# Kernel optimization log

Measured on AMD Instinct MI355X. Metric: run time of the kernel, lower is better.

The kernel has to match this reference:

```python
import jax, jax.numpy as jnp
import numpy as np

M, N, D, P = 1024, 4096, 128, 3072
H = N // D


def setup_inputs() -> dict:
    key = jax.random.key(0)
    ks = jax.random.split(key, 6)
    X = jax.random.normal(ks[0], (M, N), dtype=jnp.float32)
    W_q = jax.random.normal(ks[1], (N, N), dtype=jnp.float32) * 0.02
    W_k = jax.random.normal(ks[2], (N, N), dtype=jnp.float32) * 0.02
    W_v = jax.random.normal(ks[3], (N, N), dtype=jnp.float32) * 0.02
    cache_K = jax.random.normal(ks[4], (H, P, D), dtype=jnp.float32)
    cache_V = jax.random.normal(ks[5], (H, P, D), dtype=jnp.float32)
    return {"X": X, "W_q": W_q, "W_k": W_k, "W_v": W_v,
            "cache_K": cache_K, "cache_V": cache_V}


def _rms_norm(t):
    # RMS over last dim, no eps, no learned scale (matches source)
    var = jnp.mean(t * t, axis=-1, keepdims=True)
    return t * jax.lax.rsqrt(var)


def reference(X, W_q, W_k, W_v, cache_K, cache_V):
    # QKV projections: [M, N] -> [H, M, D]
    q = (X @ W_q).reshape(M, H, D).transpose(1, 0, 2)
    k = (X @ W_k).reshape(M, H, D).transpose(1, 0, 2)
    v = (X @ W_v).reshape(M, H, D).transpose(1, 0, 2)

    q = _rms_norm(q)
    k = _rms_norm(k)

    # KV-cache concat along sequence dim: [H, P+M, D]
    k_cache = jnp.concatenate([cache_K[:, :P, :], k], axis=1)
    v_cache = jnp.concatenate([cache_V[:, :P, :], v], axis=1)

    # Non-causal prefill attention, sm_scale = 1.0
    scores = jnp.einsum('hmd,hnd->hmn', q, k_cache)  # [H, M, P+M]
    attn = jax.nn.softmax(scores, axis=-1)
    out = jnp.einsum('hmn,hnd->hmd', attn, v_cache)  # [H, M, D]

    return out.transpose(1, 0, 2).reshape(M, N)
```

## Files before the change

kernel.cpp:

```cpp
#include <hip/hip_runtime.h>

#define MM 1024
#define NN 4096
#define DD 128
#define HH 32
#define PP 3072
#define LL 4096

typedef __attribute__((ext_vector_type(8))) short short8;
typedef __attribute__((ext_vector_type(4))) float f32x4;

__device__ __forceinline__ float bf2f(short b) {
  union { unsigned u; float f; } c;
  c.u = ((unsigned)(unsigned short)b) << 16;
  return c.f;
}

__device__ __forceinline__ short f2bf(float f) {
  union { float f; unsigned u; } c; c.f = f;
  unsigned r = c.u + 0x7FFFu + ((c.u >> 16) & 1u);
  return (short)(r >> 16);
}

struct bf2 { short hi, lo; };
__device__ __forceinline__ bf2 split2(float x) {
  bf2 r;
  r.hi = f2bf(x);
  r.lo = f2bf(x - bf2f(r.hi));
  return r;
}

__device__ __forceinline__ short8 cvt8(const float* __restrict__ p) {
  const f32x4 a = *(const f32x4*)p;
  const f32x4 b = *(const f32x4*)(p + 4);
  short8 r;
  r[0] = f2bf(a[0]); r[1] = f2bf(a[1]); r[2] = f2bf(a[2]); r[3] = f2bf(a[3]);
  r[4] = f2bf(b[0]); r[5] = f2bf(b[1]); r[6] = f2bf(b[2]); r[7] = f2bf(b[3]);
  return r;
}

__global__ __launch_bounds__(256) void split_x(
    const float* __restrict__ in, short* __restrict__ oh,
    short* __restrict__ ol, int n8)
{
  int i = blockIdx.x * blockDim.x + threadIdx.x;
  if (i >= n8) return;
  const float* p = in + (size_t)i * 8;
  f32x4 a = *(const f32x4*)p, b = *(const f32x4*)(p + 4);
  short8 h, l;
  #pragma unroll
  for (int j = 0; j < 4; ++j) {
    bf2 ra = split2(a[j]); h[j] = ra.hi; l[j] = ra.lo;
    bf2 rb = split2(b[j]); h[4 + j] = rb.hi; l[4 + j] = rb.lo;
  }
  *(short8*)(oh + (size_t)i * 8) = h;
  *(short8*)(ol + (size_t)i * 8) = l;
}

__global__ __launch_bounds__(256) void gemm_qk_split(
    const short* __restrict__ Xhi, const short* __restrict__ Xlo,
    const float* __restrict__ Wq, const float* __restrict__ Wk,
    float* __restrict__ Oq, float* __restrict__ Ok)
{
  const int z = blockIdx.z;
  const float* __restrict__ W = (z == 0) ? Wq : Wk;
  float* __restrict__ O = (z == 0) ? Oq : Ok;

  const int n0 = blockIdx.x * 128;
  const int m0 = blockIdx.y * 128;
  const int t  = threadIdx.x;
  const int wave = t >> 6;
  const int lane = t & 63;
  const int ln   = lane & 15;
  const int quad = lane >> 4;
  const int q8   = quad * 8;
  const int wm = (wave >> 1) * 64;
  const int wn = (wave & 1) * 64;

  __shared__ short Ah[128 * 72];
  __shared__ short Al[128 * 72];
  __shared__ short Bh[64 * 136];
  __shared__ short Bl[64 * 136];

  f32x4 acc[4][4];
  #pragma unroll
  for (int mi = 0; mi < 4; ++mi)
    #pragma unroll
    for (int ni = 0; ni < 4; ++ni)
      acc[mi][ni] = (f32x4){0.f, 0.f, 0.f, 0.f};

  const int ar = t >> 3, ac = (t & 7) * 8;
  const int bk = t >> 4, bn = (t & 15) * 8;

  for (int kt = 0; kt < 4096; kt += 64) {
    #pragma unroll
    for (int i = 0; i < 4; ++i) {
      int r = i * 32 + ar;
      size_t off = (size_t)(m0 + r) * 4096 + kt + ac;
      *(short8*)(Ah + r * 72 + ac) = *(const short8*)(Xhi + off);
      *(short8*)(Al + r * 72 + ac) = *(const short8*)(Xlo + off);
    }
    #pragma unroll
    for (int i = 0; i < 4; ++i) {
      int kr = i * 16 + bk;
      const float* wp = W + (size_t)(kt + kr) * 4096 + n0 + bn;
      f32x4 x0 = *(const f32x4*)wp, x1 = *(const f32x4*)(wp + 4);
      short8 hh, ll;
      #pragma unroll
      for (int j = 0; j < 4; ++j) {
        bf2 r0 = split2(x0[j]); hh[j] = r0.hi; ll[j] = r0.lo;
        bf2 r1 = split2(x1[j]); hh[4 + j] = r1.hi; ll[4 + j] = r1.lo;
      }
      int cb = (bn >> 3) ^ (kr >> 3);
      *(short8*)(Bh + kr * 136 + cb * 8) = hh;
      *(short8*)(Bl + kr * 136 + cb * 8) = ll;
    }
    __syncthreads();
    #pragma unroll
    for (int kk = 0; kk < 64; kk += 32) {
      short8 afh[4], afl[4];
      #pragma unroll
      for (int mi = 0; mi < 4; ++mi) {
        int ro = (wm + mi * 16 + ln) * 72 + kk + q8;
        afh[mi] = *(const short8*)(Ah + ro);
        afl[mi] = *(const short8*)(Al + ro);
      }
      #pragma unroll
      for (int ni = 0; ni < 4; ++ni) {
        short8 bh, bl;
        #pragma unroll
        for (int j = 0; j < 8; ++j) {
          int k = kk + q8 + j;
          int idx = k * 136 + ((((wn + ni * 16 + ln) >> 3) ^ (k >> 3)) << 3) + (ln & 7);
          bh[j] = Bh[idx];
          bl[j] = Bl[idx];
        }
        #pragma unroll
        for (int mi = 0; mi < 4; ++mi) {
          acc[mi][ni] = __builtin_amdgcn_mfma_f32_16x16x32_bf16(afh[mi], bh, acc[mi][ni], 0, 0, 0);
          acc[mi][ni] = __builtin_amdgcn_mfma_f32_16x16x32_bf16(afh[mi], bl, acc[mi][ni], 0, 0, 0);
          acc[mi][ni] = __builtin_amdgcn_mfma_f32_16x16x32_bf16(afl[mi], bh, acc[mi][ni], 0, 0, 0);
        }
      }
    }
    __syncthreads();
  }

  #pragma unroll
  for (int mi = 0; mi < 4; ++mi)
    #pragma unroll
    for (int ni = 0; ni < 4; ++ni)
      #pragma unroll
      for (int r = 0; r < 4; ++r) {
        int row = m0 + wm + mi * 16 + quad * 4 + r;
        int col = n0 + wn + ni * 16 + ln;
        O[(size_t)row * 4096 + col] = acc[mi][ni][r];
      }
}

__global__ __launch_bounds__(256) void gemm_v(
    const short* __restrict__ Xhi, const float* __restrict__ Wv,
    short* __restrict__ Ov)
{
  const int n0 = blockIdx.x * 128;
  const int m0 = blockIdx.y * 128;
  const int t  = threadIdx.x;
  const int wave = t >> 6;
  const int lane = t & 63;
  const int ln   = lane & 15;
  const int quad = lane >> 4;
  const int q8   = quad * 8;
  const int wm = (wave >> 1) * 64;
  const int wn = (wave & 1) * 64;

  __shared__ short Ah[128 * 72];
  __shared__ short Bh[64 * 136];

  f32x4 acc[4][4];
  #pragma unroll
  for (int mi = 0; mi < 4; ++mi)
    #pragma unroll
    for (int ni = 0; ni < 4; ++ni)
      acc[mi][ni] = (f32x4){0.f, 0.f, 0.f, 0.f};

  const int ar = t >> 3, ac = (t & 7) * 8;
  const int bk = t >> 4, bn = (t & 15) * 8;

  for (int kt = 0; kt < 4096; kt += 64) {
    #pragma unroll
    for (int i = 0; i < 4; ++i) {
      int r = i * 32 + ar;
      *(short8*)(Ah + r * 72 + ac) =
          *(const short8*)(Xhi + (size_t)(m0 + r) * 4096 + kt + ac);
    }
    #pragma unroll
    for (int i = 0; i < 4; ++i) {
      int kr = i * 16 + bk;
      int cb = (bn >> 3) ^ (kr >> 3);
      *(short8*)(Bh + kr * 136 + cb * 8) =
          cvt8(Wv + (size_t)(kt + kr) * 4096 + n0 + bn);
    }
    __syncthreads();
    #pragma unroll
    for (int kk = 0; kk < 64; kk += 32) {
      short8 afh[4];
      #pragma unroll
      for (int mi = 0; mi < 4; ++mi)
        afh[mi] = *(const short8*)(Ah + (wm + mi * 16 + ln) * 72 + kk + q8);
      #pragma unroll
      for (int ni = 0; ni < 4; ++ni) {
        short8 bh;
        #pragma unroll
        for (int j = 0; j < 8; ++j) {
          int k = kk + q8 + j;
          int idx = k * 136 + ((((wn + ni * 16 + ln) >> 3) ^ (k >> 3)) << 3) + (ln & 7);
          bh[j] = Bh[idx];
        }
        #pragma unroll
        for (int mi = 0; mi < 4; ++mi)
          acc[mi][ni] = __builtin_amdgcn_mfma_f32_16x16x32_bf16(afh[mi], bh, acc[mi][ni], 0, 0, 0);
      }
    }
    __syncthreads();
  }

  #pragma unroll
  for (int mi = 0; mi < 4; ++mi)
    #pragma unroll
    for (int ni = 0; ni < 4; ++ni)
      #pragma unroll
      for (int r = 0; r < 4; ++r) {
        int row = m0 + wm + mi * 16 + quad * 4 + r;
        int col = n0 + wn + ni * 16 + ln;
        Ov[(size_t)row * 4096 + col] = f2bf(acc[mi][ni][r]);
      }
}

__global__ __launch_bounds__(256) void rmsnorm_f32(
    float* __restrict__ Q, float* __restrict__ K)
{
  float* __restrict__ buf = (blockIdx.y == 0) ? Q : K;
  const int m = blockIdx.x;
  const int t = threadIdx.x;
  const int head = t >> 3, li = t & 7;
  size_t base = (size_t)m * 4096 + head * 128 + li * 16;

  f32x4 a[4];
  float ss = 0.f;
  #pragma unroll
  for (int i = 0; i < 4; ++i) {
    a[i] = *(const f32x4*)(buf + base + i * 4);
    #pragma unroll
    for (int j = 0; j < 4; ++j) ss += a[i][j] * a[i][j];
  }
  #pragma unroll
  for (int d = 1; d < 8; d <<= 1) ss += __shfl_xor(ss, d, 64);
  float scale = rsqrtf(ss * (1.0f / 128.0f));
  #pragma unroll
  for (int i = 0; i < 4; ++i) {
    #pragma unroll
    for (int j = 0; j < 4; ++j) a[i][j] *= scale;
    *(f32x4*)(buf + base + i * 4) = a[i];
  }
}

__global__ __launch_bounds__(256) void attn(
    const float* __restrict__ Qf,
    const float* __restrict__ Kf,
    const short* __restrict__ Vb,
    const float* __restrict__ cK,
    const float* __restrict__ cV,
    float* __restrict__ Out)
{
  const int h  = blockIdx.y;
  const int m0 = blockIdx.x * 64;
  const int t  = threadIdx.x;
  const int w    = t >> 6;
  const int lane = t & 63;
  const int ln   = lane & 15;
  const int quad = lane >> 4;
  const int q8   = quad * 8;

  __shared__ short k_hi[64 * 136];
  __shared__ short k_lo[64 * 136];
  __shared__ short v_s[64 * 136];
  __shared__ short p_s[64 * 72];
  __shared__ float a_l[64], l_l[64];

  short8 qh[4], ql[4];
  {
    int qrow = m0 + w * 16 + ln;
    #pragma unroll
    for (int dc = 0; dc < 4; ++dc) {
      const float* qp = Qf + (size_t)qrow * 4096 + h * 128 + dc * 32 + q8;
      f32x4 a = *(const f32x4*)qp, b = *(const f32x4*)(qp + 4);
      #pragma unroll
      for (int j = 0; j < 4; ++j) {
        bf2 ra = split2(a[j]); qh[dc][j] = ra.hi; ql[dc][j] = ra.lo;
        bf2 rb = split2(b[j]); qh[dc][4 + j] = rb.hi; ql[dc][4 + j] = rb.lo;
      }
    }
  }

  float m_st[4], l_st[4];
  #pragma unroll
  for (int r = 0; r < 4; ++r) { m_st[r] = -1e30f; l_st[r] = 0.f; }

  f32x4 oacc[4][2];
  #pragma unroll
  for (int ms = 0; ms < 4; ++ms)
    #pragma unroll
    for (int i = 0; i < 2; ++i)
      oacc[ms][i] = (f32x4){0.f, 0.f, 0.f, 0.f};

  for (int kb = 0; kb < LL; kb += 64) {
    #pragma unroll
    for (int i = 0; i < 2; ++i) {
      int kr = i * 32 + (t >> 3);
      int g  = kb + kr;
      int dc = (t & 7) * 16;
      const float* ks = (g < PP)
          ? cK + ((size_t)h * PP + g) * 128 + dc
          : Kf + (size_t)(g - PP) * 4096 + h * 128 + dc;
      f32x4 x0 = *(const f32x4*)ks,       x1 = *(const f32x4*)(ks + 4);
      f32x4 x2 = *(const f32x4*)(ks + 8), x3 = *(const f32x4*)(ks + 12);
      short8 h0, l0, h1, l1;
      #pragma unroll
      for (int j = 0; j < 4; ++j) {
        bf2 r0 = split2(x0[j]); h0[j] = r0.hi; l0[j] = r0.lo;
        bf2 r1 = split2(x1[j]); h0[4 + j] = r1.hi; l0[4 + j] = r1.lo;
        bf2 r2 = split2(x2[j]); h1[j] = r2.hi; l1[j] = r2.lo;
        bf2 r3 = split2(x3[j]); h1[4 + j] = r3.hi; l1[4 + j] = r3.lo;
      }
      *(short8*)(k_hi + kr * 136 + dc)     = h0;
      *(short8*)(k_hi + kr * 136 + dc + 8) = h1;
      *(short8*)(k_lo + kr * 136 + dc)     = l0;
      *(short8*)(k_lo + kr * 136 + dc + 8) = l1;

      short8 v0, v1;
      if (g < PP) {
        const float* vs = cV + ((size_t)h * PP + g) * 128 + dc;
        v0 = cvt8(vs); v1 = cvt8(vs + 8);
      } else {
        const short* vp = Vb + (size_t)(g - PP) * 4096 + h * 128 + dc;
        v0 = *(const short8*)vp; v1 = *(const short8*)(vp + 8);
      }
      int b0 = ((dc >> 3) + 0) ^ (kr >> 3);
      int b1 = ((dc >> 3) + 1) ^ (kr >> 3);
      *(short8*)(v_s + kr * 136 + b0 * 8) = v0;
      *(short8*)(v_s + kr * 136 + b1 * 8) = v1;
    }
    __syncthreads();

    f32x4 sacc[4];
    #pragma unroll
    for (int ni = 0; ni < 4; ++ni) sacc[ni] = (f32x4){0.f, 0.f, 0.f, 0.f};
    #pragma unroll
    for (int ni = 0; ni < 4; ++ni) {
      #pragma unroll
      for (int dc = 0; dc < 4; ++dc) {
        int ro = (ni * 16 + ln) * 136 + dc * 32 + q8;
        short8 kh = *(const short8*)(k_hi + ro);
        short8 kl = *(const short8*)(k_lo + ro);
        sacc[ni] = __builtin_amdgcn_mfma_f32_16x16x32_bf16(qh[dc], kh, sacc[ni], 0, 0, 0);
        sacc[ni] = __builtin_amdgcn_mfma_f32_16x16x32_bf16(qh[dc], kl, sacc[ni], 0, 0, 0);
        sacc[ni] = __builtin_amdgcn_mfma_f32_16x16x32_bf16(ql[dc], kh, sacc[ni], 0, 0, 0);
      }
    }

    float alpha[4];
    #pragma unroll
    for (int rr = 0; rr < 4; ++rr) {
      float mx = fmaxf(fmaxf(sacc[0][rr], sacc[1][rr]),
                       fmaxf(sacc[2][rr], sacc[3][rr]));
      #pragma unroll
      for (int d = 1; d < 16; d <<= 1) mx = fmaxf(mx, __shfl_xor(mx, d, 64));
      float mn = fmaxf(m_st[rr], mx);
      alpha[rr] = __expf(m_st[rr] - mn);
      float p0 = __expf(sacc[0][rr] - mn);
      float p1 = __expf(sacc[1][rr] - mn);
      float p2 = __expf(sacc[2][rr] - mn);
      float p3 = __expf(sacc[3][rr] - mn);
      float s = p0 + p1 + p2 + p3;
      #pragma unroll
      for (int d = 1; d < 16; d <<= 1) s += __shfl_xor(s, d, 64);
      l_st[rr] = l_st[rr] * alpha[rr] + s;
      m_st[rr] = mn;
      int prow = (w * 16 + quad * 4 + rr) * 72;
      p_s[prow + 0 * 16 + ln] = f2bf(p0);
      p_s[prow + 1 * 16 + ln] = f2bf(p1);
      p_s[prow + 2 * 16 + ln] = f2bf(p2);
      p_s[prow + 3 * 16 + ln] = f2bf(p3);
    }
    if (ln == 0) {
      #pragma unroll
      for (int rr = 0; rr < 4; ++rr) a_l[w * 16 + quad * 4 + rr] = alpha[rr];
    }
    __syncthreads();

    #pragma unroll
    for (int ms = 0; ms < 4; ++ms) {
      f32x4 av = *(const f32x4*)(a_l + ms * 16 + quad * 4);
      #pragma unroll
      for (int i = 0; i < 2; ++i)
        #pragma unroll
        for (int r = 0; r < 4; ++r) oacc[ms][i][r] *= av[r];
    }
    #pragma unroll
    for (int kk = 0; kk < 64; kk += 32) {
      short8 vf[2];
      #pragma unroll
      for (int i = 0; i < 2; ++i) {
        int cbb = (w * 2 + i) * 2 + (ln >> 3);
        #pragma unroll
        for (int j = 0; j < 8; ++j) {
          int k = kk + q8 + j;
          vf[i][j] = v_s[k * 136 + ((cbb ^ (k >> 3)) << 3) + (ln & 7)];
        }
      }
      #pragma unroll
      for (int ms = 0; ms < 4; ++ms) {
        short8 pf = *(const short8*)(p_s + (ms * 16 + ln) * 72 + kk + q8);
        #pragma unroll
        for (int i = 0; i < 2; ++i)
          oacc[ms][i] = __builtin_amdgcn_mfma_f32_16x16x32_bf16(pf, vf[i], oacc[ms][i], 0, 0, 0);
      }
    }
    __syncthreads();
  }

  if (ln == 0) {
    #pragma unroll
    for (int rr = 0; rr < 4; ++rr) l_l[w * 16 + quad * 4 + rr] = l_st[rr];
  }
  __syncthreads();

  #pragma unroll
  for (int ms = 0; ms < 4; ++ms) {
    f32x4 lv = *(const f32x4*)(l_l + ms * 16 + quad * 4);
    #pragma unroll
    for (int i = 0; i < 2; ++i) {
      int col = h * 128 + (w * 2 + i) * 16 + ln;
      #pragma unroll
      for (int r = 0; r < 4; ++r) {
        int row = m0 + ms * 16 + quad * 4 + r;
        Out[(size_t)row * 4096 + col] = oacc[ms][i][r] / lv[r];
      }
    }
  }
}

extern "C" void kernel_launch(void* const* d_in, const int* in_sizes, int n_in,
                              void* d_out, int out_size, void* d_ws, size_t ws_size,
                              hipStream_t stream) {
  const float* X  = (const float*)d_in[0];
  const float* Wq = (const float*)d_in[1];
  const float* Wk = (const float*)d_in[2];
  const float* Wv = (const float*)d_in[3];
  const float* cK = (const float*)d_in[4];
  const float* cV = (const float*)d_in[5];
  float* out = (float*)d_out;

  const size_t E = (size_t)MM * NN;
  short* Xh = (short*)d_ws;
  short* Xl = Xh + E;
  short* Vb = Xl + E;
  float* Qf = (float*)(Vb + E);
  float* Kf = Qf + E;

  {
    int n8 = (int)(E / 8);
    split_x<<<n8 / 256, 256, 0, stream>>>(X, Xh, Xl, n8);
  }

  dim3 gqk(NN / 128, MM / 128, 2);
  gemm_qk_split<<<gqk, 256, 0, stream>>>(Xh, Xl, Wq, Wk, Qf, Kf);

  dim3 gv(NN / 128, MM / 128);
  gemm_v<<<gv, 256, 0, stream>>>(Xh, Wv, Vb);

  dim3 gn(MM, 2);
  rmsnorm_f32<<<gn, 256, 0, stream>>>(Qf, Kf);

  dim3 ga(MM / 64, HH);
  attn<<<ga, 256, 0, stream>>>(Qf, Kf, Vb, cK, cV, out);
}
```

Before: 1.124 ms.

## Pre-split and transpose weights to bf16, load GEMM tiles via global_load_lds

Adds a pre-pass that converts each weight matrix into transposed bf16 hi/lo halves in workspace, so the projection GEMMs stream K-contiguous bf16 tiles for both operands. The tiles now go straight into LDS through the global_load_lds builtin, and fragments for both A and B are read as vector LDS loads instead of per-element gathers. This removes the per-block repeated fp32-to-bf16 split of W and the scalar LDS reads. The cost is an extra read and write of each 64 MB weight and reuse of one workspace buffer, which serialises the three projections. The unpadded 64-wide LDS rows may also cause bank conflicts.

```diff
diff --git a/kernel.cpp b/kernel.cpp
--- a/kernel.cpp
+++ b/kernel.cpp
@@ -37,6 +37,12 @@
   r[0] = f2bf(a[0]); r[1] = f2bf(a[1]); r[2] = f2bf(a[2]); r[3] = f2bf(a[3]);
   r[4] = f2bf(b[0]); r[5] = f2bf(b[1]); r[6] = f2bf(b[2]); r[7] = f2bf(b[3]);
   return r;
+}
+
+__device__ __forceinline__ void gload16(const void* g, void* l) {
+  __builtin_amdgcn_global_load_lds(
+      (const __attribute__((address_space(1))) void*)g,
+      (__attribute__((address_space(3))) void*)l, 16, 0, 0);
 }
 
 __global__ __launch_bounds__(256) void split_x(
@@ -57,15 +63,43 @@
   *(short8*)(ol + (size_t)i * 8) = l;
 }
 
-__global__ __launch_bounds__(256) void gemm_qk_split(
-    const short* __restrict__ Xhi, const short* __restrict__ Xlo,
-    const float* __restrict__ Wq, const float* __restrict__ Wk,
-    float* __restrict__ Oq, float* __restrict__ Ok)
+__global__ __launch_bounds__(256) void split_w_t(
+    const float* __restrict__ W, short* __restrict__ oh,
+    short* __restrict__ ol)
 {
-  const int z = blockIdx.z;
-  const float* __restrict__ W = (z == 0) ? Wq : Wk;
-  float* __restrict__ O = (z == 0) ? Oq : Ok;
-
+  const int n0 = blockIdx.x * 256;
+  const int k0 = blockIdx.y * 64;
+  const int t  = threadIdx.x;
+  const int k8 = k0 + ((t >> 5) << 3);
+  const int n8 = n0 + ((t & 31) << 3);
+
+  f32x4 xa[8], xb[8];
+  #pragma unroll
+  for (int r = 0; r < 8; ++r) {
+    const float* p = W + (size_t)(k8 + r) * 4096 + n8;
+    xa[r] = *(const f32x4*)p;
+    xb[r] = *(const f32x4*)(p + 4);
+  }
+  #pragma unroll
+  for (int c = 0; c < 8; ++c) {
+    short8 th, tl;
+    #pragma unroll
+    for (int r = 0; r < 8; ++r) {
+      float v = (c < 4) ? xa[r][c] : xb[r][c - 4];
+      bf2 s = split2(v);
+      th[r] = s.hi; tl[r] = s.lo;
+    }
+    size_t o = (size_t)(n8 + c) * 4096 + k8;
+    *(short8*)(oh + o) = th;
+    if (ol) *(short8*)(ol + o) = tl;
+  }
+}
+
+__global__ __launch_bounds__(256) void gemm_split_bt(
+    const short* __restrict__ Ah_g, const short* __restrict__ Al_g,
+    const short* __restrict__ Bh_g, const short* __restrict__ Bl_g,
+    float* __restrict__ O)
+{
   const int n0 = blockIdx.x * 128;
   const int m0 = blockIdx.y * 128;
   const int t  = threadIdx.x;
@@ -76,11 +110,13 @@
   const int q8   = quad * 8;
   const int wm = (wave >> 1) * 64;
   const int wn = (wave & 1) * 64;
-
-  __shared__ short Ah[128 * 72];
-  __shared__ short Al[128 * 72];
-  __shared__ short Bh[64 * 136];
-  __shared__ short Bl[64 * 136];
+  const int sr = lane >> 3;
+  const int sc = (lane & 7) * 8;
+
+  __shared__ short Ash[128 * 64];
+  __shared__ short Asl[128 * 64];
+  __shared__ short Bsh[128 * 64];
+  __shared__ short Bsl[128 * 64];
 
   f32x4 acc[4][4];
   #pragma unroll
@@ -89,59 +125,45 @@
     for (int ni = 0; ni < 4; ++ni)
       acc[mi][ni] = (f32x4){0.f, 0.f, 0.f, 0.f};
 
-  const int ar = t >> 3, ac = (t & 7) * 8;
-  const int bk = t >> 4, bn = (t & 15) * 8;
+  const size_t a_base = (size_t)(m0 + wave * 32 + sr) * 4096 + sc;
+  const size_t b_base = (size_t)(n0 + wave * 32 + sr) * 4096 + sc;
+  const int l_base = wave * 32 * 64;
 
   for (int kt = 0; kt < 4096; kt += 64) {
     #pragma unroll
     for (int i = 0; i < 4; ++i) {
-      int r = i * 32 + ar;
-      size_t off = (size_t)(m0 + r) * 4096 + kt + ac;
-      *(short8*)(Ah + r * 72 + ac) = *(const short8*)(Xhi + off);
-      *(short8*)(Al + r * 72 + ac) = *(const short8*)(Xlo + off);
-    }
-    #pragma unroll
-    for (int i = 0; i < 4; ++i) {
-      int kr = i * 16 + bk;
-      const float* wp = W + (size_t)(kt + kr) * 4096 + n0 + bn;
-      f32x4 x0 = *(const f32x4*)wp, x1 = *(const f32x4*)(wp + 4);
-      short8 hh, ll;
-      #pragma unroll
-      for (int j = 0; j < 4; ++j) {
-        bf2 r0 = split2(x0[j]); hh[j] = r0.hi; ll[j] = r0.lo;
-        bf2 r1 = split2(x1[j]); hh[4 + j] = r1.hi; ll[4 + j] = r1.lo;
-      }
-      int cb = (bn >> 3) ^ (kr >> 3);
-      *(short8*)(Bh + kr * 136 + cb * 8) = hh;
-      *(short8*)(Bl + kr * 136 + cb * 8) = ll;
+      size_t ao = a_base + kt + (size_t)(i * 8) * 4096;
+      size_t bo = b_base + kt + (size_t)(i * 8) * 4096;
+      int lo = l_base + i * 8 * 64;
+      gload16(Ah_g + ao, Ash + lo);
+      gload16(Al_g + ao, Asl + lo);
+      gload16(Bh_g + bo, Bsh + lo);
+      gload16(Bl_g + bo, Bsl + lo);
     }
     __syncthreads();
     #pragma unroll
     for (int kk = 0; kk < 64; kk += 32) {
-      short8 afh[4], afl[4];
+      short8 ah[4], al[4], bh[4], bl[4];
       #pragma unroll
       for (int mi = 0; mi < 4; ++mi) {
-        int ro = (wm + mi * 16 + ln) * 72 + kk + q8;
-        afh[mi] = *(const short8*)(Ah + ro);
-        afl[mi] = *(const short8*)(Al + ro);
+        int ro = (wm + mi * 16 + ln) * 64 + kk + q8;
+        ah[mi] = *(const short8*)(Ash + ro);
+        al[mi] = *(const short8*)(Asl + ro);
       }
       #pragma unroll
       for (int ni = 0; ni < 4; ++ni) {
-        short8 bh, bl;
-        #pragma unroll
-        for (int j = 0; j < 8; ++j) {
-          int k = kk + q8 + j;
-          int idx = k * 136 + ((((wn + ni * 16 + ln) >> 3) ^ (k >> 3)) << 3) + (ln & 7);
-          bh[j] = Bh[idx];
-          bl[j] = Bl[idx];
-        }
+        int ro = (wn + ni * 16 + ln) * 64 + kk + q8;
+        bh[ni] = *(const short8*)(Bsh + ro);
+        bl[ni] = *(const short8*)(Bsl + ro);
+      }
+      #pragma unroll
+      for (int ni = 0; ni < 4; ++ni)
         #pragma unroll
         for (int mi = 0; mi < 4; ++mi) {
-          acc[mi][ni] = __builtin_amdgcn_mfma_f32_16x16x32_bf16(afh[mi], bh, acc[mi][ni], 0, 0, 0);
-          acc[mi][ni] = __builtin_amdgcn_mfma_f32_16x16x32_bf16(afh[mi], bl, acc[mi][ni], 0, 0, 0);
-          acc[mi][ni] = __builtin_amdgcn_mfma_f32_16x16x32_bf16(afl[mi], bh, acc[mi][ni], 0, 0, 0);
+          acc[mi][ni] = __builtin_amdgcn_mfma_f32_16x16x32_bf16(ah[mi], bh[ni], acc[mi][ni], 0, 0, 0);
+          acc[mi][ni] = __builtin_amdgcn_mfma_f32_16x16x32_bf16(ah[mi], bl[ni], acc[mi][ni], 0, 0, 0);
+          acc[mi][ni] = __builtin_amdgcn_mfma_f32_16x16x32_bf16(al[mi], bh[ni], acc[mi][ni], 0, 0, 0);
         }
-      }
     }
     __syncthreads();
   }
@@ -158,8 +180,8 @@
       }
 }
 
-__global__ __launch_bounds__(256) void gemm_v(
-    const short* __restrict__ Xhi, const float* __restrict__ Wv,
+__global__ __launch_bounds__(256) void gemm_bf16_bt(
+    const short* __restrict__ Ah_g, const short* __restrict__ Bh_g,
     short* __restrict__ Ov)
 {
   const int n0 = blockIdx.x * 128;
@@ -172,9 +194,11 @@
   const int q8   = quad * 8;
   const int wm = (wave >> 1) * 64;
   const int wn = (wave & 1) * 64;
-
-  __shared__ short Ah[128 * 72];
-  __shared__ short Bh[64 * 136];
+  const int sr = lane >> 3;
+  const int sc = (lane & 7) * 8;
+
+  __shared__ short Ash[128 * 64];
+  __shared__ short Bsh[128 * 64];
 
   f32x4 acc[4][4];
   #pragma unroll
@@ -183,43 +207,34 @@
     for (int ni = 0; ni < 4; ++ni)
       acc[mi][ni] = (f32x4){0.f, 0.f, 0.f, 0.f};
 
-  const int ar = t >> 3, ac = (t & 7) * 8;
-  const int bk = t >> 4, bn = (t & 15) * 8;
+  const size_t a_base = (size_t)(m0 + wave * 32 + sr) * 4096 + sc;
+  const size_t b_base = (size_t)(n0 + wave * 32 + sr) * 4096 + sc;
+  const int l_base = wave * 32 * 64;
 
   for (int kt = 0; kt < 4096; kt += 64) {
     #pragma unroll
     for (int i = 0; i < 4; ++i) {
-      int r = i * 32 + ar;
-      *(short8*)(Ah + r * 72 + ac) =
-          *(const short8*)(Xhi + (size_t)(m0 + r) * 4096 + kt + ac);
-    }
-    #pragma unroll
-    for (int i = 0; i < 4; ++i) {
-      int kr = i * 16 + bk;
-      int cb = (bn >> 3) ^ (kr >> 3);
-      *(short8*)(Bh + kr * 136 + cb * 8) =
-          cvt8(Wv + (size_t)(kt + kr) * 4096 + n0 + bn);
+      size_t ao = a_base + kt + (size_t)(i * 8) * 4096;
+      size_t bo = b_base + kt + (size_t)(i * 8) * 4096;
+      int lo = l_base + i * 8 * 64;
+      gload16(Ah_g + ao, Ash + lo);
+      gload16(Bh_g + bo, Bsh + lo);
     }
     __syncthreads();
     #pragma unroll
     for (int kk = 0; kk < 64; kk += 32) {
-      short8 afh[4];
+      short8 ah[4], bh[4];
       #pragma unroll
       for (int mi = 0; mi < 4; ++mi)
-        afh[mi] = *(const short8*)(Ah + (wm + mi * 16 + ln) * 72 + kk + q8);
-      #pragma unroll
-      for (int ni = 0; ni < 4; ++ni) {
-        short8 bh;
-        #pragma unroll
-        for (int j = 0; j < 8; ++j) {
-          int k = kk + q8 + j;
-          int idx = k * 136 + ((((wn + ni * 16 + ln) >> 3) ^ (k >> 3)) << 3) + (ln & 7);
-          bh[j] = Bh[idx];
-        }
+        ah[mi] = *(const short8*)(Ash + (wm + mi * 16 + ln) * 64 + kk + q8);
+      #pragma unroll
+      for (int ni = 0; ni < 4; ++ni)
+        bh[ni] = *(const short8*)(Bsh + (wn + ni * 16 + ln) * 64 + kk + q8);
+      #pragma unroll
+      for (int ni = 0; ni < 4; ++ni)
         #pragma unroll
         for (int mi = 0; mi < 4; ++mi)
-          acc[mi][ni] = __builtin_amdgcn_mfma_f32_16x16x32_bf16(afh[mi], bh, acc[mi][ni], 0, 0, 0);
-      }
+          acc[mi][ni] = __builtin_amdgcn_mfma_f32_16x16x32_bf16(ah[mi], bh[ni], acc[mi][ni], 0, 0, 0);
     }
     __syncthreads();
   }
@@ -461,23 +476,32 @@
   const float* cV = (const float*)d_in[5];
   float* out = (float*)d_out;
 
-  const size_t E = (size_t)MM * NN;
-  short* Xh = (short*)d_ws;
-  short* Xl = Xh + E;
-  short* Vb = Xl + E;
-  float* Qf = (float*)(Vb + E);
-  float* Kf = Qf + E;
+  const size_t E  = (size_t)MM * NN;
+  const size_t WE = (size_t)NN * NN;
+  short* Xh  = (short*)d_ws;
+  short* Xl  = Xh + E;
+  short* Vb  = Xl + E;
+  float* Qf  = (float*)(Vb + E);
+  float* Kf  = Qf + E;
+  short* Wth = (short*)(Kf + E);
+  short* Wtl = Wth + WE;
 
   {
     int n8 = (int)(E / 8);
     split_x<<<n8 / 256, 256, 0, stream>>>(X, Xh, Xl, n8);
   }
 
-  dim3 gqk(NN / 128, MM / 128, 2);
-  gemm_qk_split<<<gqk, 256, 0, stream>>>(Xh, Xl, Wq, Wk, Qf, Kf);
-
-  dim3 gv(NN / 128, MM / 128);
-  gemm_v<<<gv, 256, 0, stream>>>(Xh, Wv, Vb);
+  dim3 gw(NN / 256, NN / 64);
+  dim3 gg(NN / 128, MM / 128);
+
+  split_w_t<<<gw, 256, 0, stream>>>(Wq, Wth, Wtl);
+  gemm_split_bt<<<gg, 256, 0, stream>>>(Xh, Xl, Wth, Wtl, Qf);
+
+  split_w_t<<<gw, 256, 0, stream>>>(Wk, Wth, Wtl);
+  gemm_split_bt<<<gg, 256, 0, stream>>>(Xh, Xl, Wth, Wtl, Kf);
+
+  split_w_t<<<gw, 256, 0, stream>>>(Wv, Wth, nullptr);
+  gemm_bf16_bt<<<gg, 256, 0, stream>>>(Xh, Wth, Vb);
 
   dim3 gn(MM, 2);
   rmsnorm_f32<<<gn, 256, 0, stream>>>(Qf, Kf);
```

New measurement: 1.023 ms. 9.0% less time.
